# Performance work log

Measured on AMD Instinct MI355X. Metric: run time of the kernel, lower is better.

Reference implementation:

```python
import jax, jax.numpy as jnp
import numpy as np

NUM_MOLS = 16384          # num_original_mols (fixed segment count)
TOTAL_KEYS = 1048576      # total fragments in batch (~64 per molecule)
QUERY_DIM = 128
KEY_DIM = 128
HIDDEN = 128              # attention_hidden_dim


def setup_inputs() -> dict:
    key = jax.random.key(0)
    k1, k2, k3, k4, k5 = jax.random.split(key, 5)
    query_batch = jax.random.normal(k1, (NUM_MOLS, QUERY_DIM), dtype=jnp.float32)
    key_batch = jax.random.normal(k2, (TOTAL_KEYS, KEY_DIM), dtype=jnp.float32)
    WQ = jax.random.normal(k3, (HIDDEN, QUERY_DIM), dtype=jnp.float32) * 0.05
    WK = jax.random.normal(k4, (HIDDEN, KEY_DIM), dtype=jnp.float32) * 0.05
    original_mol_idx_for_keys = jnp.sort(
        jax.random.randint(k5, (TOTAL_KEYS,), 0, NUM_MOLS, dtype=jnp.int64.dtype if hasattr(jnp.int64, 'dtype') else jnp.int64)
    ).astype(jnp.int32)
    return {
        "query_batch": query_batch,
        "key_batch": key_batch,
        "WQ": WQ,
        "WK": WK,
        "original_mol_idx_for_keys": original_mol_idx_for_keys,
    }


def reference(query_batch, key_batch, WQ, WK, original_mol_idx_for_keys):
    idx = original_mol_idx_for_keys
    # Dense projections (torch Linear, no bias): x @ W^T
    Q_proj = query_batch @ WQ.T                      # [num_mols, H]
    K_proj = key_batch @ WK.T                        # [total_keys, H]
    # Gather query rows per key, elementwise dot-product score
    scores = jnp.sum(Q_proj[idx] * K_proj, axis=1) / jnp.sqrt(
        jnp.asarray(HIDDEN, dtype=K_proj.dtype)
    )                                                # [total_keys]
    # scatter_softmax over variable-length segments (stable)
    seg_max = jax.ops.segment_max(scores, idx, num_segments=NUM_MOLS)
    ex = jnp.exp(scores - seg_max[idx])
    seg_sum = jax.ops.segment_sum(ex, idx, num_segments=NUM_MOLS)
    weights = ex / seg_sum[idx]
    return (weights, scores)
```

## Files before the change

### kernel.cpp

```cpp
#include <hip/hip_runtime.h>
#include <hip/hip_bf16.h>

#define QUERY_DIM 128
#define HIDDEN 128

typedef float f32x4 __attribute__((ext_vector_type(4)));

__device__ __forceinline__ float dot4(f32x4 a, f32x4 b) {
    return a.x * b.x + a.y * b.y + a.z * b.z + a.w * b.w;
}

__global__ __launch_bounds__(256) void combo_kernel(const float* __restrict__ WQ,
                                                    const float* __restrict__ WK,
                                                    float* __restrict__ W,
                                                    const int* __restrict__ idx,
                                                    int* __restrict__ start,
                                                    int nmols, int total) {
    int b = blockIdx.x;
    int t = threadIdx.x;
    if (b < 64) {
        int e = b * 2 + (t >> 7);
        int d = t & 127;
        float acc = 0.f;
#pragma unroll 8
        for (int h = 0; h < HIDDEN; ++h) {
            acc += WQ[h * QUERY_DIM + e] * WK[h * 128 + d];
        }
        W[e * 128 + d] = acc;
    } else {
        int m = (b - 64) * 256 + t;
        if (m > nmols) return;
        if (m == nmols) { start[m] = total; return; }
        int lo = 0, hi = total;
        while (lo < hi) {
            int mid = (lo + hi) >> 1;
            if (idx[mid] < m) lo = mid + 1; else hi = mid;
        }
        start[m] = lo;
    }
}

__global__ __launch_bounds__(256) void qproj_kernel(const float* __restrict__ Q,
                                                    const float* __restrict__ W,
                                                    float* __restrict__ R, int nmols) {
    __shared__ float wl[64 * 128];
    __shared__ float ql[16 * 128];
    int t = threadIdx.x;
    int c = t & 127;
    int g = t >> 7;
    long row0 = (long)blockIdx.x * 16;

    for (int i = t * 4; i < 16 * 128; i += 256 * 4) {
        *(float4*)&ql[i] = *(const float4*)&Q[row0 * QUERY_DIM + i];
    }

    float acc[8] = {0.f, 0.f, 0.f, 0.f, 0.f, 0.f, 0.f, 0.f};

    for (int half = 0; half < 2; ++half) {
        __syncthreads();
        for (int i = t * 4; i < 64 * 128; i += 256 * 4) {
            *(float4*)&wl[i] = *(const float4*)&W[half * 64 * 128 + i];
        }
        __syncthreads();
        for (int d = 0; d < 64; d += 4) {
            float w0 = wl[(d + 0) * 128 + c];
            float w1 = wl[(d + 1) * 128 + c];
            float w2 = wl[(d + 2) * 128 + c];
            float w3 = wl[(d + 3) * 128 + c];
            int dg = half * 64 + d;
#pragma unroll
            for (int r = 0; r < 8; ++r) {
                f32x4 q = *(const f32x4*)&ql[(g * 8 + r) * 128 + dg];
                acc[r] += q.x * w0 + q.y * w1 + q.z * w2 + q.w * w3;
            }
        }
    }
#pragma unroll
    for (int r = 0; r < 8; ++r) {
        long row = row0 + g * 8 + r;
        if (row < nmols) R[row * 128 + c] = acc[r];
    }
}

__global__ __launch_bounds__(256) void fused_kernel(const float* __restrict__ K,
                                                    const float* __restrict__ R,
                                                    const int* __restrict__ start,
                                                    float* __restrict__ weights,
                                                    float* scores,
                                                    int nmols) {
    const int lane = threadIdx.x & 63;
    const int half = lane >> 5;
    const int hl = lane & 31;
    const int wave = (blockIdx.x * 256 + threadIdx.x) >> 6;
    const float sc = 0.08838834764831845f;

    for (int si = 0; si < 2; ++si) {
        int s = wave * 2 + si;
        if (s >= nmols) break;
        int s0 = start[s], s1 = start[s + 1];
        if (s0 >= s1) continue;

        f32x4 rfrag = *((const f32x4*)(R + (long)s * 128) + hl);

        float mx = -__builtin_inff();
        float sum = 0.f;
        int kb = s0;

        f32x4 a0, a1, a2, a3;
        bool have = (kb + 8 <= s1);
        if (have) {
            long k = kb + half;
            a0 = __builtin_nontemporal_load((const f32x4*)(K + (k + 0) * 128) + hl);
            a1 = __builtin_nontemporal_load((const f32x4*)(K + (k + 2) * 128) + hl);
            a2 = __builtin_nontemporal_load((const f32x4*)(K + (k + 4) * 128) + hl);
            a3 = __builtin_nontemporal_load((const f32x4*)(K + (k + 6) * 128) + hl);
        }
        while (have) {
            bool havenext = (kb + 16 <= s1);
            f32x4 b0, b1, b2, b3;
            if (havenext) {
                long kn = kb + 8 + half;
                b0 = __builtin_nontemporal_load((const f32x4*)(K + (kn + 0) * 128) + hl);
                b1 = __builtin_nontemporal_load((const f32x4*)(K + (kn + 2) * 128) + hl);
                b2 = __builtin_nontemporal_load((const f32x4*)(K + (kn + 4) * 128) + hl);
                b3 = __builtin_nontemporal_load((const f32x4*)(K + (kn + 6) * 128) + hl);
            }
            float v0 = dot4(a0, rfrag);
            float v1 = dot4(a1, rfrag);
            float v2 = dot4(a2, rfrag);
            float v3 = dot4(a3, rfrag);
#pragma unroll
            for (int off = 16; off > 0; off >>= 1) {
                v0 += __shfl_xor(v0, off, 64);
                v1 += __shfl_xor(v1, off, 64);
                v2 += __shfl_xor(v2, off, 64);
                v3 += __shfl_xor(v3, off, 64);
            }
            v0 *= sc; v1 *= sc; v2 *= sc; v3 *= sc;
            long k = kb + half;
            if (hl == 0) {
                scores[k + 0] = v0;
                scores[k + 2] = v1;
                scores[k + 4] = v2;
                scores[k + 6] = v3;
            }
            float bm = fmaxf(fmaxf(v0, v1), fmaxf(v2, v3));
            float nm = fmaxf(mx, bm);
            sum = sum * __expf(mx - nm)
                + __expf(v0 - nm) + __expf(v1 - nm)
                + __expf(v2 - nm) + __expf(v3 - nm);
            mx = nm;
            kb += 8;
            a0 = b0; a1 = b1; a2 = b2; a3 = b3;
            have = havenext;
        }
        for (long k = kb + half; k < s1; k += 2) {
            f32x4 kv = __builtin_nontemporal_load((const f32x4*)(K + k * 128) + hl);
            float v = dot4(kv, rfrag);
#pragma unroll
            for (int off = 16; off > 0; off >>= 1) v += __shfl_xor(v, off, 64);
            v *= sc;
            if (hl == 0) scores[k] = v;
            float nm = fmaxf(mx, v);
            sum = sum * __expf(mx - nm) + __expf(v - nm);
            mx = nm;
        }
        float mo = __shfl_xor(mx, 32, 64);
        float so = __shfl_xor(sum, 32, 64);
        float nm = fmaxf(mx, mo);
        sum = sum * __expf(mx - nm) + so * __expf(mo - nm);
        mx = nm;
        float inv = 1.0f / sum;

        asm volatile("s_waitcnt vmcnt(0)" ::: "memory");

        for (int i = s0 + lane; i < s1; i += 64)
            weights[i] = __expf(scores[i] - mx) * inv;
    }
}

extern "C" void kernel_launch(void* const* d_in, const int* in_sizes, int n_in,
                              void* d_out, int out_size, void* d_ws, size_t ws_size,
                              hipStream_t stream) {
    const float* Q   = (const float*)d_in[0];
    const float* K   = (const float*)d_in[1];
    const float* WQ  = (const float*)d_in[2];
    const float* WK  = (const float*)d_in[3];
    const int*   idx = (const int*)d_in[4];

    const int nmols = in_sizes[0] / QUERY_DIM;
    const int total = in_sizes[4];

    float* weights = (float*)d_out;
    float* scores  = (float*)d_out + total;

    char* ws = (char*)d_ws;
    float* W        = (float*)ws;
    int*   segstart = (int*)(ws + 65536);
    float* R        = (float*)(ws + 65536 + 131072);

    int segblocks = (nmols + 1 + 255) / 256;
    combo_kernel<<<64 + segblocks, 256, 0, stream>>>(WQ, WK, W, idx, segstart, nmols, total);
    qproj_kernel<<<(nmols + 15) / 16, 256, 0, stream>>>(Q, W, R, nmols);
    fused_kernel<<<2048, 256, 0, stream>>>(K, R, segstart, weights, scores, nmols);
}
```

Measured before the change: 138.5 us.

## Fuse segment search and query projection into the attention-softmax kernel

Merges the segment-boundary binary search, the Q-times-W projection, and the score/softmax pass into one kernel. Each block handles 8 molecules, computes their projected queries into shared memory, and finds segment starts locally, so the R and start arrays no longer round-trip through global memory and two launches go away. The W=WQ^T·WK product stays in its own small kernel. In exchange, every block reloads the full 64KB W matrix and runs the projection before streaming keys. Because blocks are per-molecule rather than a fixed grid, the key loads can no longer overlap with the projection work of other blocks in the same way.

Measured after the change: 242.9 us. +75.3%, slower.

```diff
diff --git a/kernel.cpp b/kernel.cpp
--- a/kernel.cpp
+++ b/kernel.cpp
@@ -10,56 +10,63 @@
     return a.x * b.x + a.y * b.y + a.z * b.z + a.w * b.w;
 }
 
-__global__ __launch_bounds__(256) void combo_kernel(const float* __restrict__ WQ,
-                                                    const float* __restrict__ WK,
-                                                    float* __restrict__ W,
-                                                    const int* __restrict__ idx,
-                                                    int* __restrict__ start,
-                                                    int nmols, int total) {
-    int b = blockIdx.x;
-    int t = threadIdx.x;
-    if (b < 64) {
-        int e = b * 2 + (t >> 7);
-        int d = t & 127;
-        float acc = 0.f;
+__global__ void wqk_kernel(const float* __restrict__ WQ,
+                           const float* __restrict__ WK,
+                           float* __restrict__ W) {
+    int e = blockIdx.x;
+    int d = threadIdx.x;
+    float acc = 0.f;
 #pragma unroll 8
-        for (int h = 0; h < HIDDEN; ++h) {
-            acc += WQ[h * QUERY_DIM + e] * WK[h * 128 + d];
-        }
-        W[e * 128 + d] = acc;
-    } else {
-        int m = (b - 64) * 256 + t;
-        if (m > nmols) return;
-        if (m == nmols) { start[m] = total; return; }
-        int lo = 0, hi = total;
-        while (lo < hi) {
-            int mid = (lo + hi) >> 1;
-            if (idx[mid] < m) lo = mid + 1; else hi = mid;
-        }
-        start[m] = lo;
-    }
-}
-
-__global__ __launch_bounds__(256) void qproj_kernel(const float* __restrict__ Q,
-                                                    const float* __restrict__ W,
-                                                    float* __restrict__ R, int nmols) {
+    for (int h = 0; h < HIDDEN; ++h) {
+        acc += WQ[h * QUERY_DIM + e] * WK[h * 128 + d];
+    }
+    W[e * 128 + d] = acc;
+}
+
+__global__ __launch_bounds__(256) void mega_kernel(const float* __restrict__ Q,
+                                                   const float* __restrict__ W,
+                                                   const float* __restrict__ K,
+                                                   const int* __restrict__ idx,
+                                                   float* __restrict__ weights,
+                                                   float* scores,
+                                                   int nmols, int total) {
     __shared__ float wl[64 * 128];
-    __shared__ float ql[16 * 128];
-    int t = threadIdx.x;
-    int c = t & 127;
-    int g = t >> 7;
-    long row0 = (long)blockIdx.x * 16;
-
-    for (int i = t * 4; i < 16 * 128; i += 256 * 4) {
-        *(float4*)&ql[i] = *(const float4*)&Q[row0 * QUERY_DIM + i];
-    }
-
-    float acc[8] = {0.f, 0.f, 0.f, 0.f, 0.f, 0.f, 0.f, 0.f};
-
-    for (int half = 0; half < 2; ++half) {
+    __shared__ float ql[8 * 128];
+    __shared__ float rbuf[8 * 128];
+    __shared__ int   segb[9];
+
+    const int t = threadIdx.x;
+    const long row0 = (long)blockIdx.x * 8;
+
+    if (t < 9) {
+        int m = (int)row0 + t;
+        if (m >= nmols) {
+            segb[t] = total;
+        } else {
+            int lo = 0, hi = total;
+            while (lo < hi) {
+                int mid = (lo + hi) >> 1;
+                if (idx[mid] < m) lo = mid + 1; else hi = mid;
+            }
+            segb[t] = lo;
+        }
+    }
+
+    {
+        long qmax = (long)nmols * 128 - 4;
+        long qoff = row0 * 128 + t * 4;
+        if (qoff > qmax) qoff = qmax;
+        *(f32x4*)&ql[t * 4] = *(const f32x4*)&Q[qoff];
+    }
+
+    const int c = t & 127;
+    const int g = t >> 7;
+    float acc[4] = {0.f, 0.f, 0.f, 0.f};
+
+    for (int hf = 0; hf < 2; ++hf) {
         __syncthreads();
         for (int i = t * 4; i < 64 * 128; i += 256 * 4) {
-            *(float4*)&wl[i] = *(const float4*)&W[half * 64 * 128 + i];
+            *(f32x4*)&wl[i] = *(const f32x4*)&W[hf * 64 * 128 + i];
         }
         __syncthreads();
         for (int d = 0; d < 64; d += 4) {
@@ -67,40 +74,32 @@
             float w1 = wl[(d + 1) * 128 + c];
             float w2 = wl[(d + 2) * 128 + c];
             float w3 = wl[(d + 3) * 128 + c];
-            int dg = half * 64 + d;
-#pragma unroll
-            for (int r = 0; r < 8; ++r) {
-                f32x4 q = *(const f32x4*)&ql[(g * 8 + r) * 128 + dg];
+            int dg = hf * 64 + d;
+#pragma unroll
+            for (int r = 0; r < 4; ++r) {
+                f32x4 q = *(const f32x4*)&ql[(g * 4 + r) * 128 + dg];
                 acc[r] += q.x * w0 + q.y * w1 + q.z * w2 + q.w * w3;
             }
         }
     }
 #pragma unroll
-    for (int r = 0; r < 8; ++r) {
-        long row = row0 + g * 8 + r;
-        if (row < nmols) R[row * 128 + c] = acc[r];
-    }
-}
-
-__global__ __launch_bounds__(256) void fused_kernel(const float* __restrict__ K,
-                                                    const float* __restrict__ R,
-                                                    const int* __restrict__ start,
-                                                    float* __restrict__ weights,
-                                                    float* scores,
-                                                    int nmols) {
-    const int lane = threadIdx.x & 63;
-    const int half = lane >> 5;
+    for (int r = 0; r < 4; ++r) rbuf[(g * 4 + r) * 128 + c] = acc[r];
+    __syncthreads();
+
+    const int lane = t & 63;
+    const int hw = lane >> 5;
     const int hl = lane & 31;
-    const int wave = (blockIdx.x * 256 + threadIdx.x) >> 6;
+    const int wv = t >> 6;
     const float sc = 0.08838834764831845f;
 
     for (int si = 0; si < 2; ++si) {
-        int s = wave * 2 + si;
+        int ls = wv * 2 + si;
+        long s = row0 + ls;
         if (s >= nmols) break;
-        int s0 = start[s], s1 = start[s + 1];
+        int s0 = segb[ls], s1 = segb[ls + 1];
         if (s0 >= s1) continue;
 
-        f32x4 rfrag = *((const f32x4*)(R + (long)s * 128) + hl);
+        f32x4 rfrag = *(const f32x4*)&rbuf[ls * 128 + hl * 4];
 
         float mx = -__builtin_inff();
         float sum = 0.f;
@@ -109,7 +108,7 @@
         f32x4 a0, a1, a2, a3;
         bool have = (kb + 8 <= s1);
         if (have) {
-            long k = kb + half;
+            long k = kb + hw;
             a0 = __builtin_nontemporal_load((const f32x4*)(K + (k + 0) * 128) + hl);
             a1 = __builtin_nontemporal_load((const f32x4*)(K + (k + 2) * 128) + hl);
             a2 = __builtin_nontemporal_load((const f32x4*)(K + (k + 4) * 128) + hl);
@@ -119,7 +118,7 @@
             bool havenext = (kb + 16 <= s1);
             f32x4 b0, b1, b2, b3;
             if (havenext) {
-                long kn = kb + 8 + half;
+                long kn = kb + 8 + hw;
                 b0 = __builtin_nontemporal_load((const f32x4*)(K + (kn + 0) * 128) + hl);
                 b1 = __builtin_nontemporal_load((const f32x4*)(K + (kn + 2) * 128) + hl);
                 b2 = __builtin_nontemporal_load((const f32x4*)(K + (kn + 4) * 128) + hl);
@@ -137,7 +136,7 @@
                 v3 += __shfl_xor(v3, off, 64);
             }
             v0 *= sc; v1 *= sc; v2 *= sc; v3 *= sc;
-            long k = kb + half;
+            long k = kb + hw;
             if (hl == 0) {
                 scores[k + 0] = v0;
                 scores[k + 2] = v1;
@@ -154,7 +153,7 @@
             a0 = b0; a1 = b1; a2 = b2; a3 = b3;
             have = havenext;
         }
-        for (long k = kb + half; k < s1; k += 2) {
+        for (long k = kb + hw; k < s1; k += 2) {
             f32x4 kv = __builtin_nontemporal_load((const f32x4*)(K + k * 128) + hl);
             float v = dot4(kv, rfrag);
 #pragma unroll
@@ -194,13 +193,9 @@
     float* weights = (float*)d_out;
     float* scores  = (float*)d_out + total;
 
-    char* ws = (char*)d_ws;
-    float* W        = (float*)ws;
-    int*   segstart = (int*)(ws + 65536);
-    float* R        = (float*)(ws + 65536 + 131072);
-
-    int segblocks = (nmols + 1 + 255) / 256;
-    combo_kernel<<<64 + segblocks, 256, 0, stream>>>(WQ, WK, W, idx, segstart, nmols, total);
-    qproj_kernel<<<(nmols + 15) / 16, 256, 0, stream>>>(Q, W, R, nmols);
-    fused_kernel<<<2048, 256, 0, stream>>>(K, R, segstart, weights, scores, nmols);
-}
+    float* W = (float*)d_ws;
+
+    wqk_kernel<<<128, 128, 0, stream>>>(WQ, WK, W);
+    int blocks = (nmols + 7) / 8;
+    mega_kernel<<<blocks, 256, 0, stream>>>(Q, W, K, idx, weights, scores, nmols, total);
+}
```

## Fuse query projection into segment attention kernel, dropping separate qproj launch

Applied to the files above, without the earlier changes.

Removes the standalone query-projection kernel and the intermediate R buffer. Each wave now computes its two molecules' projected query rows directly from Q and the combined WQ^T·WK matrix before streaming keys. This saves a launch and the round trip of R through global memory. In exchange every wave re-reads the 64KB W matrix (mostly from cache) and does serial projection work before its key loop starts.

Measured after the change: 158.5 us. 14.4% more time.

```diff
diff --git a/kernel.cpp b/kernel.cpp
--- a/kernel.cpp
+++ b/kernel.cpp
@@ -40,67 +40,54 @@
     }
 }
 
-__global__ __launch_bounds__(256) void qproj_kernel(const float* __restrict__ Q,
-                                                    const float* __restrict__ W,
-                                                    float* __restrict__ R, int nmols) {
-    __shared__ float wl[64 * 128];
-    __shared__ float ql[16 * 128];
-    int t = threadIdx.x;
-    int c = t & 127;
-    int g = t >> 7;
-    long row0 = (long)blockIdx.x * 16;
+__global__ __launch_bounds__(256) void fused2_kernel(const float* __restrict__ Q,
+                                                     const float* __restrict__ W,
+                                                     const float* __restrict__ K,
+                                                     const int* __restrict__ start,
+                                                     float* __restrict__ weights,
+                                                     float* scores,
+                                                     int nmols, int total) {
+    const int t = threadIdx.x;
+    const int lane = t & 63;
+    const int hw = lane >> 5;
+    const int hl = lane & 31;
+    const long wave = (blockIdx.x * 256 + t) >> 6;
+    const float sc = 0.08838834764831845f;
 
-    for (int i = t * 4; i < 16 * 128; i += 256 * 4) {
-        *(float4*)&ql[i] = *(const float4*)&Q[row0 * QUERY_DIM + i];
+    long sA = wave * 2;
+    if (sA >= nmols) return;
+    long sB = sA + 1;
+    long sBc = sB < nmols ? sB : sA;
+    int b0 = start[sA];
+    int b1 = start[sA + 1];
+    int b2 = start[sB < nmols ? sB + 1 : sB];
+
+    f32x4 r0 = {0.f, 0.f, 0.f, 0.f};
+    f32x4 r1 = {0.f, 0.f, 0.f, 0.f};
+    {
+        const float* q0 = Q + sA * 128;
+        const float* q1 = Q + sBc * 128;
+#pragma unroll 8
+        for (int d = 0; d < 128; d += 4) {
+            f32x4 qv0 = *(const f32x4*)(q0 + d);
+            f32x4 qv1 = *(const f32x4*)(q1 + d);
+            const float* wp = W + (long)d * 128 + hl * 4;
+            f32x4 w0 = *(const f32x4*)(wp);
+            f32x4 w1 = *(const f32x4*)(wp + 128);
+            f32x4 w2 = *(const f32x4*)(wp + 256);
+            f32x4 w3 = *(const f32x4*)(wp + 384);
+            r0 += qv0.x * w0 + qv0.y * w1 + qv0.z * w2 + qv0.w * w3;
+            r1 += qv1.x * w0 + qv1.y * w1 + qv1.z * w2 + qv1.w * w3;
+        }
     }
 
-    float acc[8] = {0.f, 0.f, 0.f, 0.f, 0.f, 0.f, 0.f, 0.f};
-
-    for (int half = 0; half < 2; ++half) {
-        __syncthreads();
-        for (int i = t * 4; i < 64 * 128; i += 256 * 4) {
-            *(float4*)&wl[i] = *(const float4*)&W[half * 64 * 128 + i];
-        }
-        __syncthreads();
-        for (int d = 0; d < 64; d += 4) {
-            float w0 = wl[(d + 0) * 128 + c];
-            float w1 = wl[(d + 1) * 128 + c];
-            float w2 = wl[(d + 2) * 128 + c];
-            float w3 = wl[(d + 3) * 128 + c];
-            int dg = half * 64 + d;
-#pragma unroll
-            for (int r = 0; r < 8; ++r) {
-                f32x4 q = *(const f32x4*)&ql[(g * 8 + r) * 128 + dg];
-                acc[r] += q.x * w0 + q.y * w1 + q.z * w2 + q.w * w3;
-            }
-        }
-    }
-#pragma unroll
-    for (int r = 0; r < 8; ++r) {
-        long row = row0 + g * 8 + r;
-        if (row < nmols) R[row * 128 + c] = acc[r];
-    }
-}
-
-__global__ __launch_bounds__(256) void fused_kernel(const float* __restrict__ K,
-                                                    const float* __restrict__ R,
-                                                    const int* __restrict__ start,
-                                                    float* __restrict__ weights,
-                                                    float* scores,
-                                                    int nmols) {
-    const int lane = threadIdx.x & 63;
-    const int half = lane >> 5;
-    const int hl = lane & 31;
-    const int wave = (blockIdx.x * 256 + threadIdx.x) >> 6;
-    const float sc = 0.08838834764831845f;
-
     for (int si = 0; si < 2; ++si) {
-        int s = wave * 2 + si;
+        long s = sA + si;
         if (s >= nmols) break;
-        int s0 = start[s], s1 = start[s + 1];
+        int s0 = si ? b1 : b0;
+        int s1 = si ? b2 : b1;
         if (s0 >= s1) continue;
-
-        f32x4 rfrag = *((const f32x4*)(R + (long)s * 128) + hl);
+        f32x4 rfrag = si ? r1 : r0;
 
         float mx = -__builtin_inff();
         float sum = 0.f;
@@ -109,7 +96,7 @@
         f32x4 a0, a1, a2, a3;
         bool have = (kb + 8 <= s1);
         if (have) {
-            long k = kb + half;
+            long k = kb + hw;
             a0 = __builtin_nontemporal_load((const f32x4*)(K + (k + 0) * 128) + hl);
             a1 = __builtin_nontemporal_load((const f32x4*)(K + (k + 2) * 128) + hl);
             a2 = __builtin_nontemporal_load((const f32x4*)(K + (k + 4) * 128) + hl);
@@ -117,13 +104,13 @@
         }
         while (have) {
             bool havenext = (kb + 16 <= s1);
-            f32x4 b0, b1, b2, b3;
+            f32x4 b0v, b1v, b2v, b3v;
             if (havenext) {
-                long kn = kb + 8 + half;
-                b0 = __builtin_nontemporal_load((const f32x4*)(K + (kn + 0) * 128) + hl);
-                b1 = __builtin_nontemporal_load((const f32x4*)(K + (kn + 2) * 128) + hl);
-                b2 = __builtin_nontemporal_load((const f32x4*)(K + (kn + 4) * 128) + hl);
-                b3 = __builtin_nontemporal_load((const f32x4*)(K + (kn + 6) * 128) + hl);
+                long kn = kb + 8 + hw;
+                b0v = __builtin_nontemporal_load((const f32x4*)(K + (kn + 0) * 128) + hl);
+                b1v = __builtin_nontemporal_load((const f32x4*)(K + (kn + 2) * 128) + hl);
+                b2v = __builtin_nontemporal_load((const f32x4*)(K + (kn + 4) * 128) + hl);
+                b3v = __builtin_nontemporal_load((const f32x4*)(K + (kn + 6) * 128) + hl);
             }
             float v0 = dot4(a0, rfrag);
             float v1 = dot4(a1, rfrag);
@@ -137,7 +124,7 @@
                 v3 += __shfl_xor(v3, off, 64);
             }
             v0 *= sc; v1 *= sc; v2 *= sc; v3 *= sc;
-            long k = kb + half;
+            long k = kb + hw;
             if (hl == 0) {
                 scores[k + 0] = v0;
                 scores[k + 2] = v1;
@@ -151,10 +138,10 @@
                 + __expf(v2 - nm) + __expf(v3 - nm);
             mx = nm;
             kb += 8;
-            a0 = b0; a1 = b1; a2 = b2; a3 = b3;
+            a0 = b0v; a1 = b1v; a2 = b2v; a3 = b3v;
             have = havenext;
         }
-        for (long k = kb + half; k < s1; k += 2) {
+        for (long k = kb + hw; k < s1; k += 2) {
             f32x4 kv = __builtin_nontemporal_load((const f32x4*)(K + k * 128) + hl);
             float v = dot4(kv, rfrag);
 #pragma unroll
@@ -197,10 +184,8 @@
     char* ws = (char*)d_ws;
     float* W        = (float*)ws;
     int*   segstart = (int*)(ws + 65536);
-    float* R        = (float*)(ws + 65536 + 131072);
 
     int segblocks = (nmols + 1 + 255) / 256;
     combo_kernel<<<64 + segblocks, 256, 0, stream>>>(WQ, WK, W, idx, segstart, nmols, total);
-    qproj_kernel<<<(nmols + 15) / 16, 256, 0, stream>>>(Q, W, R, nmols);
-    fused_kernel<<<2048, 256, 0, stream>>>(K, R, segstart, weights, scores, nmols);
+    fused2_kernel<<<2048, 256, 0, stream>>>(Q, W, K, segstart, weights, scores, nmols, total);
 }
```
